# Kernel tuning notes

Hardware: AMD Instinct MI355X
Metric: run time of the kernel (lower is better)

The kernel has to match this reference:

```python
import jax, jax.numpy as jnp
import numpy as np

B, S, E, H = 4, 2048, 512, 8
D = E // H  # 64 per-head dim


def setup_inputs() -> dict:
    key = jax.random.key(0)
    kq, kk, kv, kwq, kwk, kwv, kwf, kbf = jax.random.split(key, 8)
    sc = 0.02
    return {
        "query": jax.random.normal(kq, (B, S, E), dtype=jnp.float32),
        "key": jax.random.normal(kk, (B, S, E), dtype=jnp.float32),
        "value": jax.random.normal(kv, (B, S, E), dtype=jnp.float32),
        "Wq": jax.random.normal(kwq, (D, D), dtype=jnp.float32) * sc,
        "Wk": jax.random.normal(kwk, (D, D), dtype=jnp.float32) * sc,
        "Wv": jax.random.normal(kwv, (D, D), dtype=jnp.float32) * sc,
        "Wfc": jax.random.normal(kwf, (E, E), dtype=jnp.float32) * sc,
        "bfc": jnp.zeros((E,), dtype=jnp.float32),
        "mask": jnp.tril(jnp.ones((1, 1, S, S), dtype=jnp.int32)),
    }


def reference(query, key, value, Wq, Wk, Wv, Wfc, bfc, mask):
    b, qlen, _ = query.shape
    klen = key.shape[1]
    # split heads: (B, L, H, D)
    q = query.reshape(b, qlen, H, D)
    k = key.reshape(b, klen, H, D)
    v = value.reshape(b, klen, H, D)
    # per-head linear projections (torch Linear: x @ W.T, no bias)
    q = jnp.einsum('bqhd,ed->bqhe', q, Wq)
    k = jnp.einsum('bkhd,ed->bkhe', k, Wk)
    v = jnp.einsum('bkhd,ed->bkhe', v, Wv)
    # full score matrix (B, H, Q, K)
    scores = jnp.einsum('bqhd,bkhd->bhqk', q, k)
    # faithful to source: mask-fill BEFORE dividing by sqrt(d)
    scores = jnp.where(mask == 0, jnp.float32(-1e20), scores)
    scores = scores / jnp.float32(np.sqrt(D))
    attn = jax.nn.softmax(scores, axis=-1)
    out = jnp.einsum('bhqk,bkhd->bqhd', attn, v).reshape(b, qlen, H * D)
    return out @ Wfc.T + bfc
```

## Files before the change

### kernel.cpp

```cpp
#include <hip/hip_runtime.h>
#include <hip/hip_bf16.h>

#define S_LEN 2048
#define EMB 512
#define NH 8
#define HD 64

#define AS1 __attribute__((address_space(1)))
#define AS3 __attribute__((address_space(3)))

typedef __bf16 bf16x8 __attribute__((ext_vector_type(8)));
typedef __bf16 bf16x4 __attribute__((ext_vector_type(4)));
typedef float f32x4 __attribute__((ext_vector_type(4)));
typedef float f32x16 __attribute__((ext_vector_type(16)));
typedef int i32x4 __attribute__((ext_vector_type(4)));

__device__ __forceinline__ unsigned swz(unsigned byteoff, unsigned row) {
    return byteoff ^ ((row & 7u) << 4);
}

__device__ __forceinline__ void plswap(int& a, int& b) {
#if __has_builtin(__builtin_amdgcn_permlane32_swap)
    auto r = __builtin_amdgcn_permlane32_swap(a, b, false, false);
    a = r[0];
    b = r[1];
#else
    asm("v_permlane32_swap_b32 %0, %1" : "+v"(a), "+v"(b));
#endif
}

__device__ __forceinline__ bf16x8 cvt8(const float* src) {
    float4 f0 = *reinterpret_cast<const float4*>(src);
    float4 f1 = *reinterpret_cast<const float4*>(src + 4);
    bf16x8 r;
    r[0] = (__bf16)f0.x; r[1] = (__bf16)f0.y; r[2] = (__bf16)f0.z; r[3] = (__bf16)f0.w;
    r[4] = (__bf16)f1.x; r[5] = (__bf16)f1.y; r[6] = (__bf16)f1.z; r[7] = (__bf16)f1.w;
    return r;
}

__global__ __launch_bounds__(256) void wcvt_kernel(
    const float* __restrict__ Wfc, const float* __restrict__ Wq,
    const float* __restrict__ Wk, const float* __restrict__ Wv,
    __bf16* __restrict__ Wb, __bf16* __restrict__ Wf)
{
    if (blockIdx.x < 128) {
        int i = (blockIdx.x * 256 + threadIdx.x) * 8;
        *reinterpret_cast<bf16x8*>(Wb + i) = cvt8(Wfc + i);
    } else {
        int s = (blockIdx.x - 128) * 256 + threadIdx.x;
        int p = s >> 9, rem = s & 511;
        int sub = rem >> 6, l = rem & 63;
        int nf = sub >> 1, ks = sub & 1;
        int col = l & 15, g = l >> 4;
        const float* Wsrc = (p == 0) ? Wq : (p == 1) ? Wk : Wv;
        *reinterpret_cast<bf16x8*>(Wf + (size_t)s * 8) =
            cvt8(Wsrc + (nf * 16 + col) * HD + ks * 32 + g * 8);
    }
}

__global__ __launch_bounds__(256) void proj_kernel(
    const float* __restrict__ qin, const float* __restrict__ kin, const float* __restrict__ vin,
    const __bf16* __restrict__ Wf,
    __bf16* __restrict__ Qp, __bf16* __restrict__ Kf, __bf16* __restrict__ Vf)
{
    __shared__ alignas(16) unsigned char xb[3][8192];
    __shared__ alignas(16) unsigned char tb[8192];
    const int bh = blockIdx.y;
    const int b = bh >> 3, h = bh & 7;
    const int sblk = blockIdx.x << 6;
    const int tid = threadIdx.x;
    const int w = tid >> 6, l = tid & 63;
    const int col = l & 15, g = l >> 4;
    const float K1 = 0.18033688011112042f;

    const float* srcs[3] = {qin, kin, vin};
    #pragma unroll
    for (int p = 0; p < 3; ++p) {
        const float* src = srcs[p] + ((size_t)b * S_LEN + sblk) * EMB + h * HD;
        #pragma unroll
        for (int it = 0; it < 4; ++it) {
            int c = tid + it * 256;
            int row = c >> 4, c4 = c & 15;
            float4 f = *reinterpret_cast<const float4*>(src + (size_t)row * EMB + c4 * 4);
            bf16x4 t;
            t[0] = (__bf16)f.x; t[1] = (__bf16)f.y; t[2] = (__bf16)f.z; t[3] = (__bf16)f.w;
            *reinterpret_cast<bf16x4*>(&xb[p][swz(row * 128 + c4 * 8, row)]) = t;
        }
    }
    __syncthreads();

    #pragma unroll
    for (int p = 0; p < 3; ++p) {
        bf16x8 wf[4][2];
        {
            const __bf16* wfb = Wf + p * 4096 + l * 8;
            #pragma unroll
            for (int nf = 0; nf < 4; ++nf)
                #pragma unroll
                for (int ks = 0; ks < 2; ++ks)
                    wf[nf][ks] = *reinterpret_cast<const bf16x8*>(wfb + (nf * 2 + ks) * 512);
        }
        int arow = w * 16 + col;
        bf16x8 a0 = *reinterpret_cast<const bf16x8*>(&xb[p][swz(arow * 128 + g * 16, arow)]);
        bf16x8 a1 = *reinterpret_cast<const bf16x8*>(&xb[p][swz(arow * 128 + 64 + g * 16, arow)]);
        f32x4 acc[4];
        #pragma unroll
        for (int nf = 0; nf < 4; ++nf) acc[nf] = (f32x4){0.f, 0.f, 0.f, 0.f};
        #pragma unroll
        for (int nf = 0; nf < 4; ++nf) {
            acc[nf] = __builtin_amdgcn_mfma_f32_16x16x32_bf16(a0, wf[nf][0], acc[nf], 0, 0, 0);
            acc[nf] = __builtin_amdgcn_mfma_f32_16x16x32_bf16(a1, wf[nf][1], acc[nf], 0, 0, 0);
        }
        const float s0 = (p == 0) ? K1 : 1.0f;
        #pragma unroll
        for (int nf = 0; nf < 4; ++nf)
            #pragma unroll
            for (int r = 0; r < 4; ++r) {
                int srow = w * 16 + g * 4 + r;
                unsigned tba = (unsigned)(srow * 128 + (nf * 16 + col) * 2) ^ ((srow & 7u) << 4);
                *reinterpret_cast<__bf16*>(&tb[tba]) = (__bf16)(acc[nf][r] * s0);
            }
        __syncthreads();
        if (p == 0) {
            int row = tid >> 2, eb = (tid & 3) * 32;
            bf16x8 v0 = *reinterpret_cast<const bf16x8*>(&tb[(unsigned)(row * 128 + eb) ^ ((row & 7u) << 4)]);
            bf16x8 v1 = *reinterpret_cast<const bf16x8*>(&tb[(unsigned)(row * 128 + eb + 16) ^ ((row & 7u) << 4)]);
            __bf16* dp = Qp + ((size_t)bh * S_LEN + sblk + row) * HD + eb / 2;
            *reinterpret_cast<bf16x8*>(dp) = v0;
            *reinterpret_cast<bf16x8*>(dp + 8) = v1;
        } else if (p == 1) {
            #pragma unroll
            for (int it = 0; it < 2; ++it) {
                int s = tid + it * 256;
                int Tloc = s >> 8, ks = (s >> 6) & 3, li = s & 63;
                int c32 = li & 31, h2 = li >> 5;
                int row = Tloc * 32 + c32;
                unsigned tba = (unsigned)(row * 128 + ks * 32 + h2 * 16) ^ ((row & 7u) << 4);
                bf16x8 v = *reinterpret_cast<const bf16x8*>(&tb[tba]);
                *reinterpret_cast<bf16x8*>(
                    Kf + (size_t)bh * 131072 +
                    ((size_t)(blockIdx.x * 2 + Tloc) * 4 + ks) * 512 + li * 8) = v;
            }
        } else {
            #pragma unroll
            for (int it = 0; it < 2; ++it) {
                int s = tid + it * 256;
                int Tloc = s >> 8, sub = (s >> 6) & 3, li = s & 63;
                int nf = sub >> 1, ks2 = sub & 1;
                int c32 = li & 31, h2 = li >> 5;
                int dcol = nf * 32 + c32;
                bf16x8 v;
                #pragma unroll
                for (int e = 0; e < 8; ++e) {
                    int row = Tloc * 32 + ks2 * 16 + h2 * 8 + e;
                    unsigned tba = (unsigned)(row * 128 + dcol * 2) ^ ((row & 7u) << 4);
                    v[e] = *reinterpret_cast<const __bf16*>(&tb[tba]);
                }
                *reinterpret_cast<bf16x8*>(
                    Vf + (size_t)bh * 131072 +
                    ((size_t)(blockIdx.x * 2 + Tloc) * 4 + sub) * 512 + li * 8) = v;
            }
        }
        __syncthreads();
    }
}

__global__ __launch_bounds__(256, 4) void attn_kernel(
    const __bf16* __restrict__ Qp, const __bf16* __restrict__ Kf,
    const __bf16* __restrict__ Vf, __bf16* __restrict__ Oa)
{
    __shared__ float mg[4608];
    const int l_id = blockIdx.x;
    const int bh = l_id & 31;
    const int qt = 31 - (l_id >> 5);
    const int b = bh >> 3, h = bh & 7;
    const int tid = threadIdx.x;
    const int w = tid >> 6, l = tid & 63;
    const int qh = w >> 1, kh = w & 1;
    const int c32 = l & 31, hi = l >> 5;

    bf16x8 qf[4];
    {
        const __bf16* qb =
            Qp + ((size_t)bh * S_LEN + qt * 64 + qh * 32 + c32) * HD + hi * 8;
        #pragma unroll
        for (int ks = 0; ks < 4; ++ks) qf[ks] = *reinterpret_cast<const bf16x8*>(qb + ks * 16);
    }
    f32x16 oacc[2];
    #pragma unroll
    for (int nf = 0; nf < 2; ++nf)
        #pragma unroll
        for (int r = 0; r < 16; ++r) oacc[nf][r] = 0.f;
    float m = -1e30f, lsum = 0.f;

    const int cnt = (kh == 0) ? (qt + 1) : (qt + qh);
    const bool has_mask = (kh == qh);
    const __bf16* kp = Kf + (size_t)bh * 131072 + (size_t)kh * 2048 + l * 8;
    const __bf16* vp = Vf + (size_t)bh * 131072 + (size_t)kh * 2048 + l * 8;

    #pragma unroll 1
    for (int i = 0; i < cnt; ++i) {
        f32x16 sfa;
        #pragma unroll
        for (int r = 0; r < 16; ++r) sfa[r] = 0.f;
        #pragma unroll
        for (int ks = 0; ks < 4; ++ks) {
            bf16x8 kf = *reinterpret_cast<const bf16x8*>(kp + ks * 512);
            sfa = __builtin_amdgcn_mfma_f32_32x32x16_bf16(kf, qf[ks], sfa, 0, 0, 0);
        }
        if (has_mask && i == cnt - 1) {
            #pragma unroll
            for (int r = 0; r < 16; ++r) {
                int kvloc = (r & 3) + 8 * (r >> 2) + 4 * hi;
                if (kvloc > c32) sfa[r] = -1e30f;
            }
        }
        float rmax = fmaxf(fmaxf(sfa[0], sfa[1]), sfa[2]);
        rmax = fmaxf(rmax, fmaxf(sfa[3], sfa[4]));
        rmax = fmaxf(rmax, fmaxf(sfa[5], sfa[6]));
        rmax = fmaxf(rmax, fmaxf(sfa[7], sfa[8]));
        rmax = fmaxf(rmax, fmaxf(sfa[9], sfa[10]));
        rmax = fmaxf(rmax, fmaxf(sfa[11], sfa[12]));
        rmax = fmaxf(rmax, fmaxf(sfa[13], sfa[14]));
        rmax = fmaxf(rmax, sfa[15]);
        {
            int ra = __float_as_int(rmax), rb = ra;
            plswap(ra, rb);
            rmax = fmaxf(rmax, __int_as_float((l < 32) ? rb : ra));
        }
        if (__any(rmax > m + 8.0f)) {
            float mn = fmaxf(m, rmax);
            float sc = __builtin_exp2f(m - mn);
            m = mn;
            lsum *= sc;
            #pragma unroll
            for (int nf = 0; nf < 2; ++nf)
                #pragma unroll
                for (int r = 0; r < 16; ++r) oacc[nf][r] *= sc;
        }
        float rsum = 0.f;
        int wds[8];
        #pragma unroll
        for (int i2 = 0; i2 < 8; ++i2) {
            float p0 = __builtin_exp2f(sfa[2 * i2] - m);
            float p1 = __builtin_exp2f(sfa[2 * i2 + 1] - m);
            rsum += p0 + p1;
            asm("v_cvt_pk_bf16_f32 %0, %1, %2" : "=v"(wds[i2]) : "v"(p0), "v"(p1));
        }
        lsum += rsum;
        plswap(wds[0], wds[2]);
        plswap(wds[1], wds[3]);
        plswap(wds[4], wds[6]);
        plswap(wds[5], wds[7]);
        #pragma unroll
        for (int nf = 0; nf < 2; ++nf) {
            #pragma unroll
            for (int ks2 = 0; ks2 < 2; ++ks2) {
                i32x4 pw;
                pw[0] = wds[ks2 * 4 + 0];
                pw[1] = wds[ks2 * 4 + 1];
                pw[2] = wds[ks2 * 4 + 2];
                pw[3] = wds[ks2 * 4 + 3];
                bf16x8 pfk = *reinterpret_cast<bf16x8*>(&pw);
                bf16x8 vf = *reinterpret_cast<const bf16x8*>(vp + (nf * 2 + ks2) * 512);
                oacc[nf] = __builtin_amdgcn_mfma_f32_32x32x16_bf16(vf, pfk, oacc[nf], 0, 0, 0);
            }
        }
        kp += 4096;
        vp += 4096;
    }

    if (kh == 1) {
        #pragma unroll
        for (int nf = 0; nf < 2; ++nf)
            #pragma unroll
            for (int r = 0; r < 16; ++r)
                mg[qh * 2048 + (nf * 16 + r) * 64 + l] = oacc[nf][r];
        mg[4096 + qh * 128 + l] = m;
        mg[4352 + qh * 128 + l] = lsum;
    }
    __syncthreads();
    if (kh == 0) {
        float mB = mg[4096 + qh * 128 + l];
        float lB = mg[4352 + qh * 128 + l];
        float M = fmaxf(m, mB);
        float eA = __builtin_exp2f(m - M);
        float eB = __builtin_exp2f(mB - M);
        lsum = eA * lsum + eB * lB;
        #pragma unroll
        for (int nf = 0; nf < 2; ++nf)
            #pragma unroll
            for (int r = 0; r < 16; ++r)
                oacc[nf][r] = eA * oacc[nf][r] + eB * mg[qh * 2048 + (nf * 16 + r) * 64 + l];
        lsum += __shfl_xor(lsum, 32);
        float inv = 1.0f / lsum;
        const int q = qt * 64 + qh * 32 + c32;
        __bf16* op = Oa + ((size_t)b * S_LEN + q) * EMB + h * HD;
        #pragma unroll
        for (int nf = 0; nf < 2; ++nf)
            #pragma unroll
            for (int rq = 0; rq < 4; ++rq) {
                bf16x4 o4;
                #pragma unroll
                for (int e = 0; e < 4; ++e) o4[e] = (__bf16)(oacc[nf][rq * 4 + e] * inv);
                *reinterpret_cast<bf16x4*>(op + nf * 32 + rq * 8 + hi * 4) = o4;
            }
    }
}

__global__ __launch_bounds__(512) void fc_kernel(
    const __bf16* __restrict__ A,
    const __bf16* __restrict__ Wb,
    const float* __restrict__ bfc,
    float* __restrict__ out)
{
    __shared__ alignas(16) unsigned char smem[65536];
    const int tid = threadIdx.x;
    const int w = tid >> 6, l = tid & 63;
    const int c32 = l & 31, hi = l >> 5;
    const int mw = w >> 2, nw = w & 3;
    const int r0 = blockIdx.x * 128, n0 = blockIdx.y * 128;

    int sro[2], sof[2];
    #pragma unroll
    for (int j = 0; j < 2; ++j) {
        int s = w * 128 + j * 64 + l;
        int row = s >> 3, off = (s & 7) * 16;
        sro[j] = row;
        sof[j] = off ^ ((row & 7) << 4);
    }
    const unsigned char* Ag = reinterpret_cast<const unsigned char*>(A) + (size_t)r0 * 1024;
    const unsigned char* Wg = reinterpret_cast<const unsigned char*>(Wb) + (size_t)n0 * 1024;

    f32x16 oacc[2];
    #pragma unroll
    for (int nf = 0; nf < 2; ++nf)
        #pragma unroll
        for (int r = 0; r < 16; ++r) oacc[nf][r] = 0.f;

    #pragma unroll
    for (int j = 0; j < 2; ++j) {
        __builtin_amdgcn_global_load_lds(
            (const AS1 unsigned int*)(Ag + (size_t)sro[j] * 1024 + sof[j]),
            (AS3 unsigned int*)(smem + w * 2048 + j * 1024), 16, 0, 0);
        __builtin_amdgcn_global_load_lds(
            (const AS1 unsigned int*)(Wg + (size_t)sro[j] * 1024 + sof[j]),
            (AS3 unsigned int*)(smem + 16384 + w * 2048 + j * 1024), 16, 0, 0);
    }
    __syncthreads();

    int cur = 0;
    #pragma unroll 1
    for (int kc = 0; kc < 8; ++kc) {
        if (kc + 1 < 8) {
            unsigned char* Abn = smem + (cur ^ 1) * 32768;
            #pragma unroll
            for (int j = 0; j < 2; ++j) {
                __builtin_amdgcn_global_load_lds(
                    (const AS1 unsigned int*)(Ag + (size_t)sro[j] * 1024 + (kc + 1) * 128 + sof[j]),
                    (AS3 unsigned int*)(Abn + w * 2048 + j * 1024), 16, 0, 0);
                __builtin_amdgcn_global_load_lds(
                    (const AS1 unsigned int*)(Wg + (size_t)sro[j] * 1024 + (kc + 1) * 128 + sof[j]),
                    (AS3 unsigned int*)(Abn + 16384 + w * 2048 + j * 1024), 16, 0, 0);
            }
        }
        unsigned char* Ab = smem + cur * 32768;
        unsigned char* Wbuf = Ab + 16384;
        const int brow = nw * 32 + c32;
        #pragma unroll
        for (int ks = 0; ks < 4; ++ks) {
            bf16x8 bfg = *reinterpret_cast<const bf16x8*>(
                Wbuf + swz(brow * 128 + ks * 32 + hi * 16, brow));
            #pragma unroll
            for (int nf = 0; nf < 2; ++nf) {
                int arow = mw * 64 + nf * 32 + c32;
                bf16x8 afg = *reinterpret_cast<const bf16x8*>(
                    Ab + swz(arow * 128 + ks * 32 + hi * 16, arow));
                oacc[nf] = __builtin_amdgcn_mfma_f32_32x32x16_bf16(afg, bfg, oacc[nf], 0, 0, 0);
            }
        }
        __syncthreads();
        cur ^= 1;
    }

    const float bias = bfc[n0 + nw * 32 + c32];
    const int ncol = n0 + nw * 32 + c32;
    #pragma unroll
    for (int nf = 0; nf < 2; ++nf)
        #pragma unroll
        for (int r = 0; r < 16; ++r) {
            int mrow = r0 + mw * 64 + nf * 32 + (r & 3) + 8 * (r >> 2) + 4 * hi;
            out[(size_t)mrow * EMB + ncol] = oacc[nf][r] + bias;
        }
}

extern "C" void kernel_launch(void* const* d_in, const int* in_sizes, int n_in,
                              void* d_out, int out_size, void* d_ws, size_t ws_size,
                              hipStream_t stream) {
    const float* q   = (const float*)d_in[0];
    const float* k   = (const float*)d_in[1];
    const float* v   = (const float*)d_in[2];
    const float* Wq  = (const float*)d_in[3];
    const float* Wk  = (const float*)d_in[4];
    const float* Wv  = (const float*)d_in[5];
    const float* Wfc = (const float*)d_in[6];
    const float* bfc = (const float*)d_in[7];
    float* out = (float*)d_out;

    char* ws = (char*)d_ws;
    const size_t SZ = (size_t)4 * NH * S_LEN * HD * sizeof(__bf16);
    __bf16* Qp = (__bf16*)(ws);
    __bf16* Kf = (__bf16*)(ws + SZ);
    __bf16* Vf = (__bf16*)(ws + 2 * SZ);
    __bf16* Oa = (__bf16*)(ws + 3 * SZ);
    __bf16* Wb = (__bf16*)(ws + 4 * SZ);
    __bf16* Wf = (__bf16*)(ws + 4 * SZ + 524288);

    wcvt_kernel<<<dim3(134), 256, 0, stream>>>(Wfc, Wq, Wk, Wv, Wb, Wf);
    proj_kernel<<<dim3(S_LEN / 64, 4 * NH), 256, 0, stream>>>(q, k, v, Wf, Qp, Kf, Vf);
    attn_kernel<<<dim3(32 * 32), 256, 0, stream>>>(Qp, Kf, Vf, Oa);
    fc_kernel<<<dim3((4 * S_LEN) / 128, EMB / 128), 512, 0, stream>>>(Oa, Wb, bfc, out);
}
```

Baseline: 80.69 us.

## Split attention work into 32-row query tiles with four-way KV split per block

Each attention block now handles a single 32-row query tile, and its four waves each take every fourth KV tile, instead of two 32-row query halves with a two-way KV split. The partial softmax states are merged through shared memory in a two-level tree reduction. The grid doubles to 2048 blocks, which should give finer load balance across the causal triangle and more parallelism per query row. The cost is extra merge passes, additional barriers, and waves with uneven iteration counts, plus reloading K/V for each query tile.

New measurement: 75.67 us. -6.2%, faster.

```diff
diff --git a/kernel.cpp b/kernel.cpp
--- a/kernel.cpp
+++ b/kernel.cpp
@@ -169,20 +169,19 @@
     const __bf16* __restrict__ Qp, const __bf16* __restrict__ Kf,
     const __bf16* __restrict__ Vf, __bf16* __restrict__ Oa)
 {
-    __shared__ float mg[4608];
+    __shared__ float mg[2][2176];
     const int l_id = blockIdx.x;
     const int bh = l_id & 31;
-    const int qt = 31 - (l_id >> 5);
+    const int qt2 = 63 - (l_id >> 5);
     const int b = bh >> 3, h = bh & 7;
     const int tid = threadIdx.x;
-    const int w = tid >> 6, l = tid & 63;
-    const int qh = w >> 1, kh = w & 1;
+    const int kh = tid >> 6;
+    const int l = tid & 63;
     const int c32 = l & 31, hi = l >> 5;
 
     bf16x8 qf[4];
     {
-        const __bf16* qb =
-            Qp + ((size_t)bh * S_LEN + qt * 64 + qh * 32 + c32) * HD + hi * 8;
+        const __bf16* qb = Qp + ((size_t)bh * S_LEN + qt2 * 32 + c32) * HD + hi * 8;
         #pragma unroll
         for (int ks = 0; ks < 4; ++ks) qf[ks] = *reinterpret_cast<const bf16x8*>(qb + ks * 16);
     }
@@ -193,8 +192,8 @@
         for (int r = 0; r < 16; ++r) oacc[nf][r] = 0.f;
     float m = -1e30f, lsum = 0.f;
 
-    const int cnt = (kh == 0) ? (qt + 1) : (qt + qh);
-    const bool has_mask = (kh == qh);
+    const int cnt = (qt2 >= kh) ? ((qt2 - kh) >> 2) + 1 : 0;
+    const bool has_mask = (kh == (qt2 & 3));
     const __bf16* kp = Kf + (size_t)bh * 131072 + (size_t)kh * 2048 + l * 8;
     const __bf16* vp = Vf + (size_t)bh * 131072 + (size_t)kh * 2048 + l * 8;
 
@@ -266,23 +265,50 @@
                 oacc[nf] = __builtin_amdgcn_mfma_f32_32x32x16_bf16(vf, pfk, oacc[nf], 0, 0, 0);
             }
         }
-        kp += 4096;
-        vp += 4096;
-    }
-
-    if (kh == 1) {
+        kp += 8192;
+        vp += 8192;
+    }
+
+    if (kh & 1) {
+        float* bp = mg[kh >> 1];
         #pragma unroll
         for (int nf = 0; nf < 2; ++nf)
             #pragma unroll
             for (int r = 0; r < 16; ++r)
-                mg[qh * 2048 + (nf * 16 + r) * 64 + l] = oacc[nf][r];
-        mg[4096 + qh * 128 + l] = m;
-        mg[4352 + qh * 128 + l] = lsum;
+                bp[(nf * 16 + r) * 64 + l] = oacc[nf][r];
+        bp[2048 + l] = m;
+        bp[2112 + l] = lsum;
+    }
+    __syncthreads();
+    if (!(kh & 1)) {
+        const float* bp = mg[kh >> 1];
+        float mB = bp[2048 + l], lB = bp[2112 + l];
+        float M = fmaxf(m, mB);
+        float eA = __builtin_exp2f(m - M);
+        float eB = __builtin_exp2f(mB - M);
+        m = M;
+        lsum = eA * lsum + eB * lB;
+        #pragma unroll
+        for (int nf = 0; nf < 2; ++nf)
+            #pragma unroll
+            for (int r = 0; r < 16; ++r)
+                oacc[nf][r] = eA * oacc[nf][r] + eB * bp[(nf * 16 + r) * 64 + l];
+    }
+    __syncthreads();
+    if (kh == 2) {
+        float* bp = mg[0];
+        #pragma unroll
+        for (int nf = 0; nf < 2; ++nf)
+            #pragma unroll
+            for (int r = 0; r < 16; ++r)
+                bp[(nf * 16 + r) * 64 + l] = oacc[nf][r];
+        bp[2048 + l] = m;
+        bp[2112 + l] = lsum;
     }
     __syncthreads();
     if (kh == 0) {
-        float mB = mg[4096 + qh * 128 + l];
-        float lB = mg[4352 + qh * 128 + l];
+        const float* bp = mg[0];
+        float mB = bp[2048 + l], lB = bp[2112 + l];
         float M = fmaxf(m, mB);
         float eA = __builtin_exp2f(m - M);
         float eB = __builtin_exp2f(mB - M);
@@ -291,10 +317,10 @@
         for (int nf = 0; nf < 2; ++nf)
             #pragma unroll
             for (int r = 0; r < 16; ++r)
-                oacc[nf][r] = eA * oacc[nf][r] + eB * mg[qh * 2048 + (nf * 16 + r) * 64 + l];
+                oacc[nf][r] = eA * oacc[nf][r] + eB * bp[(nf * 16 + r) * 64 + l];
         lsum += __shfl_xor(lsum, 32);
         float inv = 1.0f / lsum;
-        const int q = qt * 64 + qh * 32 + c32;
+        const int q = qt2 * 32 + c32;
         __bf16* op = Oa + ((size_t)b * S_LEN + q) * EMB + h * HD;
         #pragma unroll
         for (int nf = 0; nf < 2; ++nf)
@@ -418,6 +444,6 @@
 
     wcvt_kernel<<<dim3(134), 256, 0, stream>>>(Wfc, Wq, Wk, Wv, Wb, Wf);
     proj_kernel<<<dim3(S_LEN / 64, 4 * NH), 256, 0, stream>>>(q, k, v, Wf, Qp, Kf, Vf);
-    attn_kernel<<<dim3(32 * 32), 256, 0, stream>>>(Qp, Kf, Vf, Oa);
+    attn_kernel<<<dim3(64 * 32), 256, 0, stream>>>(Qp, Kf, Vf, Oa);
     fc_kernel<<<dim3((4 * S_LEN) / 128, EMB / 128), 512, 0, stream>>>(Oa, Wb, bfc, out);
 }
```
